# Kernel optimization log

Measured on AMD Instinct MI355X. Metric: run time of the kernel, lower is better.

Reference implementation:

```python
import jax, jax.numpy as jnp
import numpy as np


def setup_inputs() -> dict:
    key = jax.random.key(0)
    k1, k2, k3 = jax.random.split(key, 3)
    B, H, N, D = 4, 16, 4096, 128
    return {
        "q": jax.random.normal(k1, (B, H, N, D), dtype=jnp.float32),
        "k": jax.random.normal(k2, (B, H, N, D), dtype=jnp.float32),
        "v": jax.random.normal(k3, (B, H, N, D), dtype=jnp.float32),
    }


def reference(q, k, v):
    # Aaren-style numerically stable online-softmax linear-attention scan.
    # q, k, v: [B, H, N, D]
    scale = 1.0
    B, H, N, D = q.shape
    qs = jnp.moveaxis(q * scale, 2, 0)  # [N, B, H, D] time-major
    ks = jnp.moveaxis(k, 2, 0)
    vs = jnp.moveaxis(v, 2, 0)

    n0 = jnp.zeros((B, H, D), dtype=q.dtype)
    d0 = jnp.zeros((B, H, 1), dtype=q.dtype)
    m0 = jnp.full((B, H, 1), -jnp.inf, dtype=q.dtype)

    def step(carry, inp):
        n_p, d_p, m_p = carry
        q_t, k_t, v_t = inp
        alpha = jnp.sum(q_t * k_t, axis=-1, keepdims=True)  # [B, H, 1]
        m_t = jnp.maximum(m_p, alpha)
        exp_mdiff = jnp.exp(m_p - m_t)
        exp_adiff = jnp.exp(alpha - m_t)
        d_t = exp_mdiff * d_p + exp_adiff
        n_t = exp_mdiff * n_p + exp_adiff * v_t
        y_t = n_t / d_t
        return (n_t, d_t, m_t), y_t

    _, y = jax.lax.scan(step, (n0, d0, m0), (qs, ks, vs))  # y: [N, B, H, D]
    return jnp.moveaxis(y, 0, 2)  # [B, H, N, D]
```

## Files before the change

### kernel.cpp

```cpp
#include <hip/hip_runtime.h>
#include <math.h>

static constexpr int ROWS = 64;
static constexpr int NSEQ = 4096;
static constexpr int DIM  = 128;
static constexpr int TCH  = 64;
static constexpr int CPR  = NSEQ / TCH;
static constexpr int NCH  = ROWS * CPR;
static constexpr int GPB  = 8;

__global__ __launch_bounds__(256) void fla_k1(
    const float* __restrict__ q, const float* __restrict__ k,
    const float* __restrict__ v,
    float* __restrict__ wsAlpha, float* __restrict__ aggM,
    float* __restrict__ aggD, float* __restrict__ aggN)
{
    const int tid  = threadIdx.x;
    const int lane = tid & 31;
    const int g    = blockIdx.x * GPB + (tid >> 5);
    const int base = g * TCH * DIM;

    float m_cur = -INFINITY;
    float d_run = 0.0f;
    float4 acc  = make_float4(0.f, 0.f, 0.f, 0.f);
    float a0 = 0.f, a1 = 0.f;

    for (int t = 0; t < TCH; ++t) {
        const float4 q4 = *((const float4*)(q + base + t * DIM) + lane);
        const float4 k4 = *((const float4*)(k + base + t * DIM) + lane);
        float s = q4.x * k4.x + q4.y * k4.y + q4.z * k4.z + q4.w * k4.w;
        s += __shfl_xor(s, 16);
        s += __shfl_xor(s, 8);
        s += __shfl_xor(s, 4);
        s += __shfl_xor(s, 2);
        s += __shfl_xor(s, 1);
        a0 = (t == lane)      ? s : a0;
        a1 = (t == lane + 32) ? s : a1;
        const float m_new = fmaxf(m_cur, s);
        const float f = __expf(m_cur - m_new);
        const float w = __expf(s - m_new);
        d_run = d_run * f + w;
        const float4 v4 = *((const float4*)(v + base + t * DIM) + lane);
        acc.x = acc.x * f + w * v4.x;
        acc.y = acc.y * f + w * v4.y;
        acc.z = acc.z * f + w * v4.z;
        acc.w = acc.w * f + w * v4.w;
        m_cur = m_new;
    }

    wsAlpha[g * TCH + lane]      = a0;
    wsAlpha[g * TCH + 32 + lane] = a1;
    if (lane == 0) { aggM[g] = m_cur; aggD[g] = d_run; }
    *((float4*)(aggN + g * DIM) + lane) = acc;
}

__global__ __launch_bounds__(128) void fla_k2(
    const float* __restrict__ aggM, const float* __restrict__ aggD,
    const float* __restrict__ aggN,
    float* __restrict__ preM, float* __restrict__ preD, float* __restrict__ preN)
{
    const int r = blockIdx.x;
    const int d = threadIdx.x;
    float m = -INFINITY, dd = 0.f, n = 0.f;
    for (int c = 0; c < CPR; ++c) {
        const int g = r * CPR + c;
        if (d == 0) { preM[g] = m; preD[g] = dd; }
        preN[g * DIM + d] = n;
        const float Mc = aggM[g];
        const float Dc = aggD[g];
        const float nc = aggN[g * DIM + d];
        const float mn = fmaxf(m, Mc);
        const float f1 = __expf(m - mn);
        const float f2 = __expf(Mc - mn);
        dd = dd * f1 + Dc * f2;
        n  = n  * f1 + nc * f2;
        m  = mn;
    }
}

__global__ __launch_bounds__(256) void fla_k3(
    const float* __restrict__ v, const float* __restrict__ wsAlpha,
    const float* __restrict__ preM, const float* __restrict__ preD,
    const float* __restrict__ preN, float* __restrict__ y)
{
    const int tid  = threadIdx.x;
    const int lane = tid & 31;
    const int g    = blockIdx.x * GPB + (tid >> 5);
    const int base = g * TCH * DIM;

    const float a0 = wsAlpha[g * TCH + lane];
    const float a1 = wsAlpha[g * TCH + 32 + lane];
    float m_cur = preM[g];
    float d_run = preD[g];
    float4 acc  = *((const float4*)(preN + g * DIM) + lane);

    for (int t = 0; t < TCH; ++t) {
        const float s = __shfl((t & 32) ? a1 : a0, t & 31, 32);
        const float m_new = fmaxf(m_cur, s);
        const float f = __expf(m_cur - m_new);
        const float w = __expf(s - m_new);
        d_run = d_run * f + w;
        const float4 v4 = *((const float4*)(v + base + t * DIM) + lane);
        acc.x = acc.x * f + w * v4.x;
        acc.y = acc.y * f + w * v4.y;
        acc.z = acc.z * f + w * v4.z;
        acc.w = acc.w * f + w * v4.w;
        const float rinv = __builtin_amdgcn_rcpf(d_run);
        float4 y4;
        y4.x = acc.x * rinv;
        y4.y = acc.y * rinv;
        y4.z = acc.z * rinv;
        y4.w = acc.w * rinv;
        *((float4*)(y + base + t * DIM) + lane) = y4;
        m_cur = m_new;
    }
}

extern "C" void kernel_launch(void* const* d_in, const int* in_sizes, int n_in,
                              void* d_out, int out_size, void* d_ws, size_t ws_size,
                              hipStream_t stream) {
    const float* q = (const float*)d_in[0];
    const float* k = (const float*)d_in[1];
    const float* v = (const float*)d_in[2];
    float* y  = (float*)d_out;
    float* ws = (float*)d_ws;

    float* wsAlpha = ws;
    float* aggM    = wsAlpha + ROWS * NSEQ;
    float* aggD    = aggM + NCH;
    float* aggN    = aggD + NCH;
    float* preM    = aggN + NCH * DIM;
    float* preD    = preM + NCH;
    float* preN    = preD + NCH;

    fla_k1<<<NCH / GPB, 256, 0, stream>>>(q, k, v, wsAlpha, aggM, aggD, aggN);
    fla_k2<<<ROWS, DIM, 0, stream>>>(aggM, aggD, aggN, preM, preD, preN);
    fla_k3<<<NCH / GPB, 256, 0, stream>>>(v, wsAlpha, preM, preD, preN, y);
}
```

Baseline: 159.8 us.

## Halve chunk length, batch loads and shuffles, and scan prefix state in place

Result: slower. 244.7 us (+53.1%).

```diff
diff --git a/kernel.cpp b/kernel.cpp
--- a/kernel.cpp
+++ b/kernel.cpp
@@ -4,71 +4,82 @@
 static constexpr int ROWS = 64;
 static constexpr int NSEQ = 4096;
 static constexpr int DIM  = 128;
-static constexpr int TCH  = 64;
+static constexpr int TCH  = 32;
 static constexpr int CPR  = NSEQ / TCH;
 static constexpr int NCH  = ROWS * CPR;
 static constexpr int GPB  = 8;
+static constexpr int U    = 8;
 
-__global__ __launch_bounds__(256) void fla_k1(
+__global__ __launch_bounds__(256, 4) void fla_k1(
     const float* __restrict__ q, const float* __restrict__ k,
     const float* __restrict__ v,
     float* __restrict__ wsAlpha, float* __restrict__ aggM,
     float* __restrict__ aggD, float* __restrict__ aggN)
 {
-    const int tid  = threadIdx.x;
-    const int lane = tid & 31;
-    const int g    = blockIdx.x * GPB + (tid >> 5);
-    const int base = g * TCH * DIM;
+    const int lane = threadIdx.x & 31;
+    const int g    = blockIdx.x * GPB + (threadIdx.x >> 5);
+    const int base = g * (TCH * DIM);
 
     float m_cur = -INFINITY;
     float d_run = 0.0f;
     float4 acc  = make_float4(0.f, 0.f, 0.f, 0.f);
-    float a0 = 0.f, a1 = 0.f;
+    float aKeep = 0.f;
 
-    for (int t = 0; t < TCH; ++t) {
-        const float4 q4 = *((const float4*)(q + base + t * DIM) + lane);
-        const float4 k4 = *((const float4*)(k + base + t * DIM) + lane);
-        float s = q4.x * k4.x + q4.y * k4.y + q4.z * k4.z + q4.w * k4.w;
-        s += __shfl_xor(s, 16);
-        s += __shfl_xor(s, 8);
-        s += __shfl_xor(s, 4);
-        s += __shfl_xor(s, 2);
-        s += __shfl_xor(s, 1);
-        a0 = (t == lane)      ? s : a0;
-        a1 = (t == lane + 32) ? s : a1;
-        const float m_new = fmaxf(m_cur, s);
-        const float f = __expf(m_cur - m_new);
-        const float w = __expf(s - m_new);
-        d_run = d_run * f + w;
-        const float4 v4 = *((const float4*)(v + base + t * DIM) + lane);
-        acc.x = acc.x * f + w * v4.x;
-        acc.y = acc.y * f + w * v4.y;
-        acc.z = acc.z * f + w * v4.z;
-        acc.w = acc.w * f + w * v4.w;
-        m_cur = m_new;
+    for (int t0 = 0; t0 < TCH; t0 += U) {
+        float4 q4[U], k4[U], v4[U];
+        float  p[U];
+        #pragma unroll
+        for (int u = 0; u < U; ++u) {
+            q4[u] = *((const float4*)(q + base + (t0 + u) * DIM) + lane);
+            k4[u] = *((const float4*)(k + base + (t0 + u) * DIM) + lane);
+        }
+        #pragma unroll
+        for (int u = 0; u < U; ++u)
+            v4[u] = *((const float4*)(v + base + (t0 + u) * DIM) + lane);
+        #pragma unroll
+        for (int u = 0; u < U; ++u)
+            p[u] = q4[u].x * k4[u].x + q4[u].y * k4[u].y
+                 + q4[u].z * k4[u].z + q4[u].w * k4[u].w;
+        #pragma unroll
+        for (int m = 16; m >= 1; m >>= 1) {
+            #pragma unroll
+            for (int u = 0; u < U; ++u) p[u] += __shfl_xor(p[u], m);
+        }
+        #pragma unroll
+        for (int u = 0; u < U; ++u) {
+            const int t = t0 + u;
+            aKeep = (t == lane) ? p[u] : aKeep;
+            const float m_new = fmaxf(m_cur, p[u]);
+            const float f = __expf(m_cur - m_new);
+            const float w = __expf(p[u] - m_new);
+            d_run = d_run * f + w;
+            acc.x = acc.x * f + w * v4[u].x;
+            acc.y = acc.y * f + w * v4[u].y;
+            acc.z = acc.z * f + w * v4[u].z;
+            acc.w = acc.w * f + w * v4[u].w;
+            m_cur = m_new;
+        }
     }
 
-    wsAlpha[g * TCH + lane]      = a0;
-    wsAlpha[g * TCH + 32 + lane] = a1;
+    wsAlpha[g * TCH + lane] = aKeep;
     if (lane == 0) { aggM[g] = m_cur; aggD[g] = d_run; }
     *((float4*)(aggN + g * DIM) + lane) = acc;
 }
 
 __global__ __launch_bounds__(128) void fla_k2(
-    const float* __restrict__ aggM, const float* __restrict__ aggD,
-    const float* __restrict__ aggN,
-    float* __restrict__ preM, float* __restrict__ preD, float* __restrict__ preN)
+    float* __restrict__ aggM, float* __restrict__ aggD, float* __restrict__ aggN)
 {
     const int r = blockIdx.x;
     const int d = threadIdx.x;
     float m = -INFINITY, dd = 0.f, n = 0.f;
     for (int c = 0; c < CPR; ++c) {
         const int g = r * CPR + c;
-        if (d == 0) { preM[g] = m; preD[g] = dd; }
-        preN[g * DIM + d] = n;
         const float Mc = aggM[g];
         const float Dc = aggD[g];
         const float nc = aggN[g * DIM + d];
+        __syncthreads();
+        if (d == 0) { aggM[g] = m; aggD[g] = dd; }
+        aggN[g * DIM + d] = n;
         const float mn = fmaxf(m, Mc);
         const float f1 = __expf(m - mn);
         const float f2 = __expf(Mc - mn);
@@ -78,41 +89,45 @@
     }
 }
 
-__global__ __launch_bounds__(256) void fla_k3(
+__global__ __launch_bounds__(256, 4) void fla_k3(
     const float* __restrict__ v, const float* __restrict__ wsAlpha,
     const float* __restrict__ preM, const float* __restrict__ preD,
     const float* __restrict__ preN, float* __restrict__ y)
 {
-    const int tid  = threadIdx.x;
-    const int lane = tid & 31;
-    const int g    = blockIdx.x * GPB + (tid >> 5);
-    const int base = g * TCH * DIM;
+    const int lane = threadIdx.x & 31;
+    const int g    = blockIdx.x * GPB + (threadIdx.x >> 5);
+    const int base = g * (TCH * DIM);
 
     const float a0 = wsAlpha[g * TCH + lane];
-    const float a1 = wsAlpha[g * TCH + 32 + lane];
     float m_cur = preM[g];
     float d_run = preD[g];
     float4 acc  = *((const float4*)(preN + g * DIM) + lane);
 
-    for (int t = 0; t < TCH; ++t) {
-        const float s = __shfl((t & 32) ? a1 : a0, t & 31, 32);
-        const float m_new = fmaxf(m_cur, s);
-        const float f = __expf(m_cur - m_new);
-        const float w = __expf(s - m_new);
-        d_run = d_run * f + w;
-        const float4 v4 = *((const float4*)(v + base + t * DIM) + lane);
-        acc.x = acc.x * f + w * v4.x;
-        acc.y = acc.y * f + w * v4.y;
-        acc.z = acc.z * f + w * v4.z;
-        acc.w = acc.w * f + w * v4.w;
-        const float rinv = __builtin_amdgcn_rcpf(d_run);
-        float4 y4;
-        y4.x = acc.x * rinv;
-        y4.y = acc.y * rinv;
-        y4.z = acc.z * rinv;
-        y4.w = acc.w * rinv;
-        *((float4*)(y + base + t * DIM) + lane) = y4;
-        m_cur = m_new;
+    for (int t0 = 0; t0 < TCH; t0 += U) {
+        float4 v4[U];
+        #pragma unroll
+        for (int u = 0; u < U; ++u)
+            v4[u] = *((const float4*)(v + base + (t0 + u) * DIM) + lane);
+        #pragma unroll
+        for (int u = 0; u < U; ++u) {
+            const float s = __shfl(a0, t0 + u, 32);
+            const float m_new = fmaxf(m_cur, s);
+            const float f = __expf(m_cur - m_new);
+            const float w = __expf(s - m_new);
+            d_run = d_run * f + w;
+            acc.x = acc.x * f + w * v4[u].x;
+            acc.y = acc.y * f + w * v4[u].y;
+            acc.z = acc.z * f + w * v4[u].z;
+            acc.w = acc.w * f + w * v4[u].w;
+            const float rinv = __builtin_amdgcn_rcpf(d_run);
+            float4 y4;
+            y4.x = acc.x * rinv;
+            y4.y = acc.y * rinv;
+            y4.z = acc.z * rinv;
+            y4.w = acc.w * rinv;
+            *((float4*)(y + base + (t0 + u) * DIM) + lane) = y4;
+            m_cur = m_new;
+        }
     }
 }
 
@@ -129,11 +144,8 @@
     float* aggM    = wsAlpha + ROWS * NSEQ;
     float* aggD    = aggM + NCH;
     float* aggN    = aggD + NCH;
-    float* preM    = aggN + NCH * DIM;
-    float* preD    = preM + NCH;
-    float* preN    = preD + NCH;
 
     fla_k1<<<NCH / GPB, 256, 0, stream>>>(q, k, v, wsAlpha, aggM, aggD, aggN);
-    fla_k2<<<ROWS, DIM, 0, stream>>>(aggM, aggD, aggN, preM, preD, preN);
-    fla_k3<<<NCH / GPB, 256, 0, stream>>>(v, wsAlpha, preM, preD, preN, y);
+    fla_k2<<<ROWS, DIM, 0, stream>>>(aggM, aggD, aggN);
+    fla_k3<<<NCH / GPB, 256, 0, stream>>>(v, wsAlpha, aggM, aggD, aggN, y);
 }
```
